# Performance work log

Hardware: AMD Instinct MI355X
Metric: run time of the kernel (lower is better)

The kernel has to match this reference:

```python
import jax, jax.numpy as jnp
import numpy as np

B, N_OBJ, N_REL = 32, 16, 64
C, H, W = 1024, 50, 50
POOL, SR = 7, 2          # roi_pool_size, sampling_ratio
SPATIAL_SCALE = 1.0      # boxes are pre-scaled to fmap coords by scale_bboxes
DIMS = [1024, 1024, 512] # lin_obj_dim
IMG = 800                # square frame -> the original's h/w swap bug is a no-op


def setup_inputs() -> dict:
    key = jax.random.key(0)
    ks = jax.random.split(key, 8)
    fmap = jax.random.normal(ks[0], (B, C, H, W), dtype=jnp.float32)
    # valid boxes in image coords: x1<x2, y1<y2, inside [0, IMG]
    xy1 = jax.random.uniform(ks[1], (B, N_OBJ, 2), minval=0.0, maxval=600.0)
    wh = jax.random.uniform(ks[2], (B, N_OBJ, 2), minval=50.0, maxval=200.0)
    bboxes = jnp.concatenate([xy1, xy1 + wh], axis=-1).astype(jnp.float32)
    num_obj = jnp.full((B,), N_OBJ, dtype=jnp.int32)
    num_rels = jnp.full((B,), N_REL, dtype=jnp.int32)
    obj_pairs = jax.random.randint(ks[3], (B, N_REL, 2), 0, N_OBJ, dtype=jnp.int32)
    s1 = 1.0 / np.sqrt(DIMS[0]).astype(np.float32)
    s2 = 1.0 / np.sqrt(DIMS[1]).astype(np.float32)
    W1 = jax.random.uniform(ks[4], (DIMS[0], DIMS[1]), minval=-s1, maxval=s1, dtype=jnp.float32)
    b1 = jax.random.uniform(ks[5], (DIMS[1],), minval=-s1, maxval=s1, dtype=jnp.float32)
    W2 = jax.random.uniform(ks[6], (DIMS[1], DIMS[2]), minval=-s2, maxval=s2, dtype=jnp.float32)
    b2 = jax.random.uniform(ks[7], (DIMS[2],), minval=-s2, maxval=s2, dtype=jnp.float32)
    return dict(frame_feature_map=fmap, bboxes=bboxes, num_obj=num_obj,
                obj_pairs=obj_pairs, num_rels=num_rels,
                frame_width=IMG, frame_height=IMG,
                W1=W1, b1=b1, W2=W2, b2=b2)


def _interp_axis(coord, size):
    # torchvision RoIAlign (aligned=False) bilinear precompute along one axis
    valid = ((coord >= -1.0) & (coord <= size)).astype(coord.dtype)
    c = jnp.maximum(coord, 0.0)
    low = jnp.floor(c).astype(jnp.int32)
    at_edge = low >= size - 1
    low = jnp.minimum(low, size - 1)
    high = jnp.minimum(low + 1, size - 1)
    l = jnp.where(at_edge, 0.0, c - low.astype(coord.dtype))
    return low, high, 1.0 - l, l, valid


def roi_align(fmap, boxes, batch_idx, pool, sr, scale):
    # fmap [B,C,H,W]; boxes [R,4] (x1,y1,x2,y2); returns [R,pool,pool,C]
    _, Cc, Hc, Wc = fmap.shape
    x1, y1, x2, y2 = (boxes[:, i] * scale for i in range(4))
    roi_w = jnp.maximum(x2 - x1, 1.0)
    roi_h = jnp.maximum(y2 - y1, 1.0)
    # sample offsets (separable): bin ph, subsample iy -> ph + (iy+0.5)/sr, in bin units
    grid = (jnp.arange(pool, dtype=fmap.dtype)[:, None]
            + (jnp.arange(sr, dtype=fmap.dtype)[None, :] + 0.5) / sr).reshape(-1)  # [pool*sr]
    ys = y1[:, None] + (roi_h / pool)[:, None] * grid[None, :]  # [R, Sy]
    xs = x1[:, None] + (roi_w / pool)[:, None] * grid[None, :]  # [R, Sx]
    yl, yh, wy0, wy1, vy = _interp_axis(ys, Hc)
    xl, xh, wx0, wx1, vx = _interp_axis(xs, Wc)
    b = batch_idx[:, None, None]

    def g(yi, xi):
        # advanced indices split by ':' -> result [R, Sy, Sx, C]
        return fmap[b, :, yi[:, :, None], xi[:, None, :]]

    val = (wy0[:, :, None, None] * (wx0[:, None, :, None] * g(yl, xl)
                                    + wx1[:, None, :, None] * g(yl, xh))
           + wy1[:, :, None, None] * (wx0[:, None, :, None] * g(yh, xl)
                                      + wx1[:, None, :, None] * g(yh, xh)))
    val = val * (vy[:, :, None, None] * vx[:, None, :, None])  # out-of-range points -> 0
    R = boxes.shape[0]
    # average the sr x sr samples per bin (count = sr*sr, as in torchvision)
    return val.reshape(R, pool, sr, pool, sr, Cc).mean(axis=(2, 4))


def reference(frame_feature_map, bboxes, num_obj, obj_pairs, num_rels,
              frame_width, frame_height, W1, b1, W2, b2):
    Bn, Nmax = bboxes.shape[:2]
    # scale_bboxes -- faithful to the original (note its im_height/im_width swap)
    im_height, im_width = frame_width, frame_height
    fh, fw = frame_feature_map.shape[-2:]
    hs = fh / (im_height * 1.0)
    ws = fw / (im_width * 1.0)
    scaled = bboxes * jnp.asarray([ws, hs, ws, hs], dtype=bboxes.dtype)
    boxes = scaled.reshape(-1, 4)                              # full counts: concat == flatten
    batch_idx = jnp.repeat(jnp.arange(Bn, dtype=jnp.int32), Nmax)
    roi = roi_align(frame_feature_map, boxes, batch_idx, POOL, SR, SPATIAL_SCALE)  # [R,7,7,C]
    # lin_obj_net: Linear+ReLU stack applied on the channel (last) dim
    h = jax.nn.relu(roi @ W1 + b1)
    h = jax.nn.relu(h @ W2 + b2)                               # [R,7,7,512]
    feat = h.mean(axis=(1, 2))                                 # AvgPool2d(7x7) -> flatten: [R,512]
    # pair_features: gather two object vectors per relation and average
    obj_off = jnp.concatenate([jnp.zeros((1,), jnp.int32),
                               jnp.cumsum(num_obj)[:-1].astype(jnp.int32)])
    idx = obj_off[:, None, None] + obj_pairs                   # [B, N_REL, 2]
    f0 = feat[idx[..., 0].reshape(-1)]
    f1 = feat[idx[..., 1].reshape(-1)]
    return 0.5 * (f0 + f1)                                     # [sum(num_rels), 512]
```

## Files before the change

kernel.cpp:

```cpp
#include <hip/hip_runtime.h>

#define DEV __device__ __forceinline__

typedef unsigned short u16;
typedef short bf16x8 __attribute__((ext_vector_type(8)));
typedef float f32x4 __attribute__((ext_vector_type(4)));

#define BB    32
#define NOBJ  16
#define NREL  64
#define CCH   1024
#define FHW   50
#define HW    2500
#define NROI  512
#define MROWS 25088
#define D1    1024
#define D2    512

DEV u16 f2bf(float f) {
  unsigned u = __float_as_uint(f);
  unsigned r = (u + 0x7FFFu + ((u >> 16) & 1u)) >> 16;
  return (u16)r;
}
DEV float bf2f(u16 h) { return __uint_as_float((unsigned)h << 16); }
DEV unsigned pk(float lo, float hi) { return (unsigned)f2bf(lo) | ((unsigned)f2bf(hi) << 16); }

using gvoid = __attribute__((address_space(1))) const void;
using svoid = __attribute__((address_space(3))) void;
DEV void gl_lds16(const void* g, void* s) {
  __builtin_amdgcn_global_load_lds((gvoid*)g, (svoid*)s, 16, 0, 0);
}

__global__ __launch_bounds__(256) void k_transpose_cast(
    const float* __restrict__ in, u16* __restrict__ out, int R, int C) {
  __shared__ float tile[64][65];
  const int b = blockIdx.z;
  const int c0 = blockIdx.x * 64;
  const int r0 = blockIdx.y * 64;
  const float* inb = in + (size_t)b * R * C;
  u16* outb = out + (size_t)b * R * C;
  const int t = threadIdx.x;

  {
    const int rr = t >> 4;
    const int cq = (t & 15) * 4;
#pragma unroll
    for (int it = 0; it < 4; ++it) {
      int rl = rr + it * 16;
      int r = r0 + rl;
      int c = c0 + cq;
      if (c + 3 < C) {
        float4 v = *reinterpret_cast<const float4*>(&inb[(size_t)r * C + c]);
        tile[rl][cq + 0] = v.x; tile[rl][cq + 1] = v.y;
        tile[rl][cq + 2] = v.z; tile[rl][cq + 3] = v.w;
      } else {
#pragma unroll
        for (int j = 0; j < 4; ++j)
          tile[rl][cq + j] = (c + j < C) ? inb[(size_t)r * C + c + j] : 0.f;
      }
    }
  }
  __syncthreads();
  {
    const int c = t >> 2;
    const int rch = (t & 3) * 8;
    if (c0 + c < C) {
#pragma unroll
      for (int half = 0; half < 2; ++half) {
        int rb = rch + half * 32;
        uint4 o;
        o.x = pk(tile[rb + 0][c], tile[rb + 1][c]);
        o.y = pk(tile[rb + 2][c], tile[rb + 3][c]);
        o.z = pk(tile[rb + 4][c], tile[rb + 5][c]);
        o.w = pk(tile[rb + 6][c], tile[rb + 7][c]);
        *reinterpret_cast<uint4*>(&outb[(size_t)(c0 + c) * R + r0 + rb]) = o;
      }
    }
  }
}

DEV void acc8(const u16* p, float w, float* a) {
  uint4 v = *reinterpret_cast<const uint4*>(p);
  a[0] = fmaf(w, bf2f((u16)(v.x & 0xffffu)), a[0]);
  a[1] = fmaf(w, bf2f((u16)(v.x >> 16)), a[1]);
  a[2] = fmaf(w, bf2f((u16)(v.y & 0xffffu)), a[2]);
  a[3] = fmaf(w, bf2f((u16)(v.y >> 16)), a[3]);
  a[4] = fmaf(w, bf2f((u16)(v.z & 0xffffu)), a[4]);
  a[5] = fmaf(w, bf2f((u16)(v.z >> 16)), a[5]);
  a[6] = fmaf(w, bf2f((u16)(v.w & 0xffffu)), a[6]);
  a[7] = fmaf(w, bf2f((u16)(v.w >> 16)), a[7]);
}

__global__ __launch_bounds__(128) void k_roi_fast(
    const u16* __restrict__ fmT, const float* __restrict__ bboxes,
    const int* __restrict__ pfw, const int* __restrict__ pfh,
    u16* __restrict__ Aout) {
  const int r = blockIdx.x;
  const int py = blockIdx.y;
  const int b = r >> 4;
  const int t = threadIdx.x;
  const int c0 = t * 8;

  __shared__ int s_lo[2][14], s_hi[2][14];
  __shared__ float s_w0[2][14], s_w1[2][14], s_v[2][14];

  int axis = -1, i = 0;
  if (t < 14) { axis = 0; i = t; }
  else if (t >= 64 && t < 78) { axis = 1; i = t - 64; }
  if (axis >= 0) {
    float fwf = (float)pfw[0], fhf = (float)pfh[0];
    float hs = (float)FHW / fwf;
    float wsc = (float)FHW / fhf;
    float v1 = bboxes[r * 4 + (axis == 0 ? 1 : 0)] * (axis == 0 ? hs : wsc);
    float v2 = bboxes[r * 4 + (axis == 0 ? 3 : 2)] * (axis == 0 ? hs : wsc);
    float ext = fmaxf(v2 - v1, 1.0f);
    float g = (float)(i >> 1) + ((i & 1) ? 0.75f : 0.25f);
    float coord = v1 + (ext / 7.0f) * g;
    float valid = (coord >= -1.0f && coord <= 50.0f) ? 1.0f : 0.0f;
    float cc = fmaxf(coord, 0.0f);
    int lo = (int)floorf(cc);
    bool edge = (lo >= FHW - 1);
    lo = min(lo, FHW - 1);
    int hi = min(lo + 1, FHW - 1);
    float l = edge ? 0.0f : (cc - (float)lo);
    s_lo[axis][i] = lo; s_hi[axis][i] = hi;
    s_w0[axis][i] = 1.0f - l; s_w1[axis][i] = l; s_v[axis][i] = valid;
  }
  __syncthreads();

  const u16* bt = fmT + (size_t)b * HW * CCH + c0;

  for (int px = 0; px < 7; ++px) {
    float a[8] = {};
#pragma unroll
    for (int s = 0; s < 4; ++s) {
      int sy = s >> 1, sx = s & 1;
      int iy = py * 2 + sy, jx = px * 2 + sx;
      int yl = s_lo[0][iy], yh = s_hi[0][iy];
      int xl = s_lo[1][jx], xh = s_hi[1][jx];
      float vv = s_v[0][iy] * s_v[1][jx];
      float wy0 = s_w0[0][iy] * vv, wy1 = s_w1[0][iy] * vv;
      float wx0 = s_w0[1][jx], wx1 = s_w1[1][jx];
      acc8(bt + (size_t)(yl * FHW + xl) * CCH, wy0 * wx0, a);
      acc8(bt + (size_t)(yl * FHW + xh) * CCH, wy0 * wx1, a);
      acc8(bt + (size_t)(yh * FHW + xl) * CCH, wy1 * wx0, a);
      acc8(bt + (size_t)(yh * FHW + xh) * CCH, wy1 * wx1, a);
    }
    u16* dst = Aout + (size_t)(r * 49 + py * 7 + px) * CCH + c0;
    uint4 o;
    o.x = pk(a[0] * 0.25f, a[1] * 0.25f);
    o.y = pk(a[2] * 0.25f, a[3] * 0.25f);
    o.z = pk(a[4] * 0.25f, a[5] * 0.25f);
    o.w = pk(a[6] * 0.25f, a[7] * 0.25f);
    *reinterpret_cast<uint4*>(dst) = o;
  }
}

__global__ __launch_bounds__(64) void k_roi_slow(
    const float* __restrict__ fmap, const float* __restrict__ bboxes,
    const int* __restrict__ pfw, const int* __restrict__ pfh,
    u16* __restrict__ Aout) {
  const int r = blockIdx.x;
  const int b = r >> 4;
  const int t = threadIdx.x;
  const int c0 = (blockIdx.y * 64 + t) * 4;

  __shared__ int s_lo[2][14], s_hi[2][14];
  __shared__ float s_w0[2][14], s_w1[2][14], s_v[2][14];

  int axis = -1, i = 0;
  if (t < 14) { axis = 0; i = t; }
  else if (t >= 32 && t < 46) { axis = 1; i = t - 32; }
  if (axis >= 0) {
    float fwf = (float)pfw[0], fhf = (float)pfh[0];
    float hs = (float)FHW / fwf;
    float wsc = (float)FHW / fhf;
    float v1 = bboxes[r * 4 + (axis == 0 ? 1 : 0)] * (axis == 0 ? hs : wsc);
    float v2 = bboxes[r * 4 + (axis == 0 ? 3 : 2)] * (axis == 0 ? hs : wsc);
    float ext = fmaxf(v2 - v1, 1.0f);
    float g = (float)(i >> 1) + ((i & 1) ? 0.75f : 0.25f);
    float coord = v1 + (ext / 7.0f) * g;
    float valid = (coord >= -1.0f && coord <= 50.0f) ? 1.0f : 0.0f;
    float cc = fmaxf(coord, 0.0f);
    int lo = (int)floorf(cc);
    bool edge = (lo >= FHW - 1);
    lo = min(lo, FHW - 1);
    int hi = min(lo + 1, FHW - 1);
    float l = edge ? 0.0f : (cc - (float)lo);
    s_lo[axis][i] = lo; s_hi[axis][i] = hi;
    s_w0[axis][i] = 1.0f - l; s_w1[axis][i] = l; s_v[axis][i] = valid;
  }
  __syncthreads();

  const float* bfc = fmap + (size_t)b * CCH * HW + (size_t)c0 * HW;

  for (int bin = 0; bin < 49; ++bin) {
    int py = bin / 7, px = bin % 7;
    float a0 = 0.f, a1 = 0.f, a2 = 0.f, a3 = 0.f;
#pragma unroll
    for (int s = 0; s < 4; ++s) {
      int sy = s >> 1, sx = s & 1;
      int iy = py * 2 + sy, jx = px * 2 + sx;
      int yl = s_lo[0][iy], yh = s_hi[0][iy];
      int xl = s_lo[1][jx], xh = s_hi[1][jx];
      float vv = s_v[0][iy] * s_v[1][jx];
      float wy0 = s_w0[0][iy] * vv, wy1 = s_w1[0][iy] * vv;
      float wx0 = s_w0[1][jx], wx1 = s_w1[1][jx];
      float w00 = wy0 * wx0, w01 = wy0 * wx1, w10 = wy1 * wx0, w11 = wy1 * wx1;
      int p00 = yl * FHW + xl, p01 = yl * FHW + xh;
      int p10 = yh * FHW + xl, p11 = yh * FHW + xh;
      a0 += w00 * bfc[0 * HW + p00] + w01 * bfc[0 * HW + p01] + w10 * bfc[0 * HW + p10] + w11 * bfc[0 * HW + p11];
      a1 += w00 * bfc[1 * HW + p00] + w01 * bfc[1 * HW + p01] + w10 * bfc[1 * HW + p10] + w11 * bfc[1 * HW + p11];
      a2 += w00 * bfc[2 * HW + p00] + w01 * bfc[2 * HW + p01] + w10 * bfc[2 * HW + p10] + w11 * bfc[2 * HW + p11];
      a3 += w00 * bfc[3 * HW + p00] + w01 * bfc[3 * HW + p01] + w10 * bfc[3 * HW + p10] + w11 * bfc[3 * HW + p11];
    }
    u16* dst = Aout + (size_t)(r * 49 + bin) * CCH + c0;
    ushort4 o;
    o.x = f2bf(a0 * 0.25f); o.y = f2bf(a1 * 0.25f);
    o.z = f2bf(a2 * 0.25f); o.w = f2bf(a3 * 0.25f);
    *reinterpret_cast<ushort4*>(dst) = o;
  }
}

template <int K, int N, int OBF>
__global__ __launch_bounds__(256) void k_gemm(
    const u16* __restrict__ A, const u16* __restrict__ Bt,
    const float* __restrict__ bias, void* __restrict__ Out) {
  __shared__ alignas(16) u16 As[128 * 32];
  __shared__ alignas(16) u16 Bs[128 * 32];
  const int t = threadIdx.x;
  const int lane = t & 63, w = t >> 6;
  const int wr = w >> 1, wc = w & 1;

  const int NT = N / 128;
  const int bid = blockIdx.x;
  const int chunk = (int)(gridDim.x >> 3);
  const int swz = (bid & 7) * chunk + (bid >> 3);
  const size_t m0 = (size_t)(swz / NT) * 128;
  const int n0 = (swz % NT) * 128;

  f32x4 acc[4][4] = {};

  const int srow = t >> 2;
  const int skc = (t & 3) * 8;

  for (int ks = 0; ks < K / 32; ++ks) {
    const int k0 = ks * 32;
    if (ks) __syncthreads();
    gl_lds16(A + (m0 + srow) * K + k0 + skc, &As[(size_t)t * 8]);
    gl_lds16(A + (m0 + 64 + srow) * K + k0 + skc, &As[(size_t)(t + 256) * 8]);
    gl_lds16(Bt + (size_t)(n0 + srow) * K + k0 + skc, &Bs[(size_t)t * 8]);
    gl_lds16(Bt + (size_t)(n0 + 64 + srow) * K + k0 + skc, &Bs[(size_t)(t + 256) * 8]);
    __syncthreads();

    const int koff = (lane >> 4) * 8;
    bf16x8 av[4], bv[4];
#pragma unroll
    for (int m = 0; m < 4; ++m)
      av[m] = *reinterpret_cast<const bf16x8*>(&As[(wr * 64 + m * 16 + (lane & 15)) * 32 + koff]);
#pragma unroll
    for (int n = 0; n < 4; ++n)
      bv[n] = *reinterpret_cast<const bf16x8*>(&Bs[(wc * 64 + n * 16 + (lane & 15)) * 32 + koff]);
#pragma unroll
    for (int m = 0; m < 4; ++m)
#pragma unroll
      for (int n = 0; n < 4; ++n)
        asm("v_mfma_f32_16x16x32_bf16 %0, %1, %2, %0"
            : "+v"(acc[m][n]) : "v"(av[m]), "v"(bv[n]));
  }
  asm volatile("s_nop 7\n\ts_nop 7\n\ts_nop 7" ::);

#pragma unroll
  for (int n = 0; n < 4; ++n) {
    int col = n0 + wc * 64 + n * 16 + (lane & 15);
    float bb = bias[col];
#pragma unroll
    for (int m = 0; m < 4; ++m) {
      size_t row0 = m0 + wr * 64 + m * 16 + (lane >> 4) * 4;
#pragma unroll
      for (int qq = 0; qq < 4; ++qq) {
        float v = fmaxf(acc[m][n][qq] + bb, 0.0f);
        if (OBF) ((u16*)Out)[(row0 + qq) * N + col] = f2bf(v);
        else     ((float*)Out)[(row0 + qq) * N + col] = v;
      }
    }
  }
}

__global__ __launch_bounds__(256) void k_mean(const u16* __restrict__ H2,
                                              float* __restrict__ feat) {
  const int r = blockIdx.x;
  const int c = threadIdx.x * 2;
  float s0 = 0.f, s1 = 0.f;
#pragma unroll
  for (int qq = 0; qq < 49; ++qq) {
    unsigned v = *reinterpret_cast<const unsigned*>(&H2[((size_t)r * 49 + qq) * D2 + c]);
    s0 += bf2f((u16)(v & 0xffffu));
    s1 += bf2f((u16)(v >> 16));
  }
  feat[(size_t)r * D2 + c] = s0 * (1.0f / 49.0f);
  feat[(size_t)r * D2 + c + 1] = s1 * (1.0f / 49.0f);
}

__global__ __launch_bounds__(256) void k_pairs(
    const float* __restrict__ feat, const int* __restrict__ num_obj,
    const int* __restrict__ pairs, float* __restrict__ out) {
  int r = blockIdx.x;
  int b = r >> 6;
  int off = 0;
  for (int i = 0; i < b; ++i) off += num_obj[i];
  int g0 = off + pairs[r * 2 + 0];
  int g1 = off + pairs[r * 2 + 1];
  for (int c = threadIdx.x; c < D2; c += 256) {
    out[(size_t)r * D2 + c] = 0.5f * (feat[(size_t)g0 * D2 + c] + feat[(size_t)g1 * D2 + c]);
  }
}

extern "C" void kernel_launch(void* const* d_in, const int* in_sizes, int n_in,
                              void* d_out, int out_size, void* d_ws, size_t ws_size,
                              hipStream_t stream) {
  const float* fmap = (const float*)d_in[0];
  const float* bboxes = (const float*)d_in[1];
  const int* num_obj = (const int*)d_in[2];
  const int* obj_pairs = (const int*)d_in[3];
  const int* pfw = (const int*)d_in[5];
  const int* pfh = (const int*)d_in[6];
  const float* W1 = (const float*)d_in[7];
  const float* b1 = (const float*)d_in[8];
  const float* W2 = (const float*)d_in[9];
  const float* b2 = (const float*)d_in[10];
  float* out = (float*)d_out;

  const size_t SZ_FMT = (size_t)BB * HW * CCH * 2;
  const size_t SZ_A   = (size_t)MROWS * D1 * 2;
  const size_t SZ_H1  = (size_t)MROWS * D1 * 2;
  const size_t SZ_W1B = (size_t)D1 * D1 * 2;
  const size_t SZ_W2B = (size_t)D1 * D2 * 2;
  const size_t SZ_FEAT = (size_t)NROI * D2 * 4;

  char* ws = (char*)d_ws;
  const bool fast = ws_size >= SZ_FMT + SZ_A + SZ_H1 + SZ_W1B + SZ_W2B + SZ_FEAT;

  u16 *fmT, *A, *H1, *W1b, *W2b, *H2b;
  float *feat;
  if (fast) {
    fmT = (u16*)ws;
    A = (u16*)(ws + SZ_FMT);
    H1 = (u16*)(ws + SZ_FMT + SZ_A);
    W1b = (u16*)(ws + SZ_FMT + SZ_A + SZ_H1);
    W2b = (u16*)(ws + SZ_FMT + SZ_A + SZ_H1 + SZ_W1B);
    feat = (float*)(ws + SZ_FMT + SZ_A + SZ_H1 + SZ_W1B + SZ_W2B);
    H2b = fmT;
  } else {
    fmT = nullptr;
    A = (u16*)ws;
    H1 = (u16*)(ws + SZ_A);
    W1b = (u16*)(ws + SZ_A + SZ_H1);
    W2b = (u16*)(ws + SZ_A + SZ_H1 + SZ_W1B);
    feat = (float*)(ws + SZ_A + SZ_H1 + SZ_W1B + SZ_W2B);
    H2b = A;
  }

  k_transpose_cast<<<dim3(16, 16, 1), 256, 0, stream>>>(W1, W1b, D1, D1);
  k_transpose_cast<<<dim3(8, 16, 1), 256, 0, stream>>>(W2, W2b, D1, D2);

  if (fast) {
    k_transpose_cast<<<dim3(40, 16, BB), 256, 0, stream>>>(fmap, fmT, CCH, HW);
    k_roi_fast<<<dim3(NROI, 7), 128, 0, stream>>>(fmT, bboxes, pfw, pfh, A);
  } else {
    k_roi_slow<<<dim3(NROI, 4), 64, 0, stream>>>(fmap, bboxes, pfw, pfh, A);
  }

  k_gemm<D1, D1, 1><<<(MROWS / 128) * (D1 / 128), 256, 0, stream>>>(A, W1b, b1, (void*)H1);
  k_gemm<D1, D2, 1><<<(MROWS / 128) * (D2 / 128), 256, 0, stream>>>(H1, W2b, b2, (void*)H2b);
  k_mean<<<NROI, 256, 0, stream>>>(H2b, feat);
  k_pairs<<<BB * NREL, 256, 0, stream>>>(feat, num_obj, obj_pairs, out);
}
```

Measured before the change: 291.0 us.

## Add 256x256 double-buffered 8-wave GEMM with swizzled LDS and remove slow ROI path

Adds a new GEMM kernel with 256x256 output tiles, 8 waves, a 64-wide K step and double-buffered dynamic LDS (128 KB). The next K tile is prefetched while MFMAs run, and LDS addresses are XOR-swizzled to avoid bank conflicts. It also uses XCD-aware block remapping and setprio around the MFMA bursts. The aim is more data reuse per tile and overlap of global loads with compute in the two large GEMMs. The fallback ROI path that avoided workspace is removed, so the code now assumes the workspace is large enough.

```diff
diff --git a/kernel.cpp b/kernel.cpp
--- a/kernel.cpp
+++ b/kernel.cpp
@@ -40,7 +40,6 @@
   const float* inb = in + (size_t)b * R * C;
   u16* outb = out + (size_t)b * R * C;
   const int t = threadIdx.x;
-
   {
     const int rr = t >> 4;
     const int cq = (t & 15) * 4;
@@ -156,69 +155,119 @@
   }
 }
 
-__global__ __launch_bounds__(64) void k_roi_slow(
-    const float* __restrict__ fmap, const float* __restrict__ bboxes,
-    const int* __restrict__ pfw, const int* __restrict__ pfh,
-    u16* __restrict__ Aout) {
-  const int r = blockIdx.x;
-  const int b = r >> 4;
+template <int K, int N, int OBF>
+__global__ __launch_bounds__(512, 2) void k_gemm8(
+    const u16* __restrict__ A, const u16* __restrict__ Bt,
+    const float* __restrict__ bias, void* __restrict__ Out) {
+  extern __shared__ char smem[];
   const int t = threadIdx.x;
-  const int c0 = (blockIdx.y * 64 + t) * 4;
-
-  __shared__ int s_lo[2][14], s_hi[2][14];
-  __shared__ float s_w0[2][14], s_w1[2][14], s_v[2][14];
-
-  int axis = -1, i = 0;
-  if (t < 14) { axis = 0; i = t; }
-  else if (t >= 32 && t < 46) { axis = 1; i = t - 32; }
-  if (axis >= 0) {
-    float fwf = (float)pfw[0], fhf = (float)pfh[0];
-    float hs = (float)FHW / fwf;
-    float wsc = (float)FHW / fhf;
-    float v1 = bboxes[r * 4 + (axis == 0 ? 1 : 0)] * (axis == 0 ? hs : wsc);
-    float v2 = bboxes[r * 4 + (axis == 0 ? 3 : 2)] * (axis == 0 ? hs : wsc);
-    float ext = fmaxf(v2 - v1, 1.0f);
-    float g = (float)(i >> 1) + ((i & 1) ? 0.75f : 0.25f);
-    float coord = v1 + (ext / 7.0f) * g;
-    float valid = (coord >= -1.0f && coord <= 50.0f) ? 1.0f : 0.0f;
-    float cc = fmaxf(coord, 0.0f);
-    int lo = (int)floorf(cc);
-    bool edge = (lo >= FHW - 1);
-    lo = min(lo, FHW - 1);
-    int hi = min(lo + 1, FHW - 1);
-    float l = edge ? 0.0f : (cc - (float)lo);
-    s_lo[axis][i] = lo; s_hi[axis][i] = hi;
-    s_w0[axis][i] = 1.0f - l; s_w1[axis][i] = l; s_v[axis][i] = valid;
-  }
-  __syncthreads();
-
-  const float* bfc = fmap + (size_t)b * CCH * HW + (size_t)c0 * HW;
-
-  for (int bin = 0; bin < 49; ++bin) {
-    int py = bin / 7, px = bin % 7;
-    float a0 = 0.f, a1 = 0.f, a2 = 0.f, a3 = 0.f;
-#pragma unroll
-    for (int s = 0; s < 4; ++s) {
-      int sy = s >> 1, sx = s & 1;
-      int iy = py * 2 + sy, jx = px * 2 + sx;
-      int yl = s_lo[0][iy], yh = s_hi[0][iy];
-      int xl = s_lo[1][jx], xh = s_hi[1][jx];
-      float vv = s_v[0][iy] * s_v[1][jx];
-      float wy0 = s_w0[0][iy] * vv, wy1 = s_w1[0][iy] * vv;
-      float wx0 = s_w0[1][jx], wx1 = s_w1[1][jx];
-      float w00 = wy0 * wx0, w01 = wy0 * wx1, w10 = wy1 * wx0, w11 = wy1 * wx1;
-      int p00 = yl * FHW + xl, p01 = yl * FHW + xh;
-      int p10 = yh * FHW + xl, p11 = yh * FHW + xh;
-      a0 += w00 * bfc[0 * HW + p00] + w01 * bfc[0 * HW + p01] + w10 * bfc[0 * HW + p10] + w11 * bfc[0 * HW + p11];
-      a1 += w00 * bfc[1 * HW + p00] + w01 * bfc[1 * HW + p01] + w10 * bfc[1 * HW + p10] + w11 * bfc[1 * HW + p11];
-      a2 += w00 * bfc[2 * HW + p00] + w01 * bfc[2 * HW + p01] + w10 * bfc[2 * HW + p10] + w11 * bfc[2 * HW + p11];
-      a3 += w00 * bfc[3 * HW + p00] + w01 * bfc[3 * HW + p01] + w10 * bfc[3 * HW + p10] + w11 * bfc[3 * HW + p11];
-    }
-    u16* dst = Aout + (size_t)(r * 49 + bin) * CCH + c0;
-    ushort4 o;
-    o.x = f2bf(a0 * 0.25f); o.y = f2bf(a1 * 0.25f);
-    o.z = f2bf(a2 * 0.25f); o.w = f2bf(a3 * 0.25f);
-    *reinterpret_cast<ushort4*>(dst) = o;
+  const int lane = t & 63;
+  const int wid = t >> 6;
+  const int wr = wid >> 2, wc = wid & 3;
+
+  const int nwg = (int)gridDim.x;
+  const int orig = (int)blockIdx.x;
+  const int xcd = orig & 7, q = nwg >> 3, r = nwg & 7;
+  const int swz = (xcd < r ? xcd * (q + 1) : r * (q + 1) + (xcd - r) * q) + (orig >> 3);
+  constexpr int GN = N / 256;
+  const size_t m0 = (size_t)(swz / GN) * 256;
+  const int n0 = (swz % GN) * 256;
+
+  constexpr int NKT = K / 64;
+
+  f32x4 acc[8][4] = {};
+
+  auto stage_quarter = [&](int bufb, int k0, int qt) {
+    const u16* src = (qt < 2) ? A : Bt;
+    const size_t rbase = (qt < 2) ? m0 : (size_t)n0;
+    const int regionBase = bufb + ((qt < 2) ? 0 : 32768);
+    const int half = qt & 1;
+#pragma unroll
+    for (int c = 0; c < 2; ++c) {
+      int P = half * 16384 + c * 8192 + t * 16;
+      int L = P ^ (((P >> 9) & 1) << 5);
+      int row = L >> 7;
+      int kb = L & 127;
+      gl_lds16(src + (rbase + row) * (size_t)K + k0 + (kb >> 1),
+               smem + regionBase + P);
+    }
+  };
+  auto lda = [&](int bufb, int mrow, int kc) -> bf16x8 {
+    int L = mrow * 128 + kc * 2;
+    int P = L ^ (((L >> 9) & 1) << 5);
+    return *reinterpret_cast<const bf16x8*>(smem + bufb + P);
+  };
+  auto ldb = [&](int bufb, int nrow, int kc) -> bf16x8 {
+    int L = nrow * 128 + kc * 2;
+    int P = L ^ (((L >> 9) & 1) << 5);
+    return *reinterpret_cast<const bf16x8*>(smem + bufb + 32768 + P);
+  };
+
+#pragma unroll
+  for (int qt = 0; qt < 4; ++qt) stage_quarter(0, 0, qt);
+  if (NKT > 1) {
+#pragma unroll
+    for (int qt = 0; qt < 4; ++qt) stage_quarter(65536, 64, qt);
+  }
+  asm volatile("s_waitcnt vmcnt(0)" ::: "memory");
+  __builtin_amdgcn_s_barrier();
+
+  for (int tt = 0; tt < NKT; ++tt) {
+    const int bb = (tt & 1) ? 65536 : 0;
+    const int nb = bb ^ 65536;
+    const bool do_stage = (tt >= 1) && (tt + 1 < NKT);
+    const int k0n = (tt + 1) * 64;
+#pragma unroll
+    for (int p = 0; p < 4; ++p) {
+      const int qm = p >> 1, qn = p & 1;
+      bf16x8 av[2][4], bv[2][2];
+#pragma unroll
+      for (int ks = 0; ks < 2; ++ks) {
+        const int kc = ks * 32 + (lane >> 4) * 8;
+#pragma unroll
+        for (int m = 0; m < 4; ++m)
+          av[ks][m] = lda(bb, wr * 128 + qm * 64 + m * 16 + (lane & 15), kc);
+#pragma unroll
+        for (int n = 0; n < 2; ++n)
+          bv[ks][n] = ldb(bb, wc * 64 + qn * 32 + n * 16 + (lane & 15), kc);
+      }
+      if (do_stage && p < 2) {
+        stage_quarter(nb, k0n, p * 2 + 0);
+        stage_quarter(nb, k0n, p * 2 + 1);
+      }
+      __builtin_amdgcn_s_barrier();
+      __builtin_amdgcn_s_setprio(1);
+#pragma unroll
+      for (int ks = 0; ks < 2; ++ks)
+#pragma unroll
+        for (int m = 0; m < 4; ++m)
+#pragma unroll
+          for (int n = 0; n < 2; ++n)
+            asm("v_mfma_f32_16x16x32_bf16 %0, %1, %2, %0"
+                : "+v"(acc[qm * 4 + m][qn * 2 + n])
+                : "v"(av[ks][m]), "v"(bv[ks][n]));
+      __builtin_amdgcn_s_setprio(0);
+      if (p == 3 && tt + 1 < NKT)
+        asm volatile("s_waitcnt vmcnt(0)" ::: "memory");
+      __builtin_amdgcn_s_barrier();
+    }
+  }
+  asm volatile("s_nop 7\n\ts_nop 7\n\ts_nop 7" ::);
+
+#pragma unroll
+  for (int nf = 0; nf < 4; ++nf) {
+    const int col = n0 + wc * 64 + nf * 16 + (lane & 15);
+    const float bbv = bias[col];
+#pragma unroll
+    for (int mf = 0; mf < 8; ++mf) {
+      const size_t row0 = m0 + wr * 128 + mf * 16 + (lane >> 4) * 4;
+#pragma unroll
+      for (int qq = 0; qq < 4; ++qq) {
+        float v = fmaxf(acc[mf][nf][qq] + bbv, 0.0f);
+        if (OBF) ((u16*)Out)[(row0 + qq) * N + col] = f2bf(v);
+        else     ((float*)Out)[(row0 + qq) * N + col] = v;
+      }
+    }
   }
 }
 
@@ -231,19 +280,15 @@
   const int t = threadIdx.x;
   const int lane = t & 63, w = t >> 6;
   const int wr = w >> 1, wc = w & 1;
-
   const int NT = N / 128;
   const int bid = blockIdx.x;
   const int chunk = (int)(gridDim.x >> 3);
   const int swz = (bid & 7) * chunk + (bid >> 3);
   const size_t m0 = (size_t)(swz / NT) * 128;
   const int n0 = (swz % NT) * 128;
-
   f32x4 acc[4][4] = {};
-
   const int srow = t >> 2;
   const int skc = (t & 3) * 8;
-
   for (int ks = 0; ks < K / 32; ++ks) {
     const int k0 = ks * 32;
     if (ks) __syncthreads();
@@ -252,7 +297,6 @@
     gl_lds16(Bt + (size_t)(n0 + srow) * K + k0 + skc, &Bs[(size_t)t * 8]);
     gl_lds16(Bt + (size_t)(n0 + 64 + srow) * K + k0 + skc, &Bs[(size_t)(t + 256) * 8]);
     __syncthreads();
-
     const int koff = (lane >> 4) * 8;
     bf16x8 av[4], bv[4];
 #pragma unroll
@@ -269,7 +313,6 @@
             : "+v"(acc[m][n]) : "v"(av[m]), "v"(bv[n]));
   }
   asm volatile("s_nop 7\n\ts_nop 7\n\ts_nop 7" ::);
-
 #pragma unroll
   for (int n = 0; n < 4; ++n) {
     int col = n0 + wc * 64 + n * 16 + (lane & 15);
@@ -339,40 +382,37 @@
   const size_t SZ_FEAT = (size_t)NROI * D2 * 4;
 
   char* ws = (char*)d_ws;
-  const bool fast = ws_size >= SZ_FMT + SZ_A + SZ_H1 + SZ_W1B + SZ_W2B + SZ_FEAT;
-
   u16 *fmT, *A, *H1, *W1b, *W2b, *H2b;
   float *feat;
-  if (fast) {
-    fmT = (u16*)ws;
-    A = (u16*)(ws + SZ_FMT);
-    H1 = (u16*)(ws + SZ_FMT + SZ_A);
-    W1b = (u16*)(ws + SZ_FMT + SZ_A + SZ_H1);
-    W2b = (u16*)(ws + SZ_FMT + SZ_A + SZ_H1 + SZ_W1B);
-    feat = (float*)(ws + SZ_FMT + SZ_A + SZ_H1 + SZ_W1B + SZ_W2B);
-    H2b = fmT;
-  } else {
-    fmT = nullptr;
-    A = (u16*)ws;
-    H1 = (u16*)(ws + SZ_A);
-    W1b = (u16*)(ws + SZ_A + SZ_H1);
-    W2b = (u16*)(ws + SZ_A + SZ_H1 + SZ_W1B);
-    feat = (float*)(ws + SZ_A + SZ_H1 + SZ_W1B + SZ_W2B);
-    H2b = A;
-  }
+  fmT = (u16*)ws;
+  A = (u16*)(ws + SZ_FMT);
+  H1 = (u16*)(ws + SZ_FMT + SZ_A);
+  W1b = (u16*)(ws + SZ_FMT + SZ_A + SZ_H1);
+  W2b = (u16*)(ws + SZ_FMT + SZ_A + SZ_H1 + SZ_W1B);
+  feat = (float*)(ws + SZ_FMT + SZ_A + SZ_H1 + SZ_W1B + SZ_W2B);
+  H2b = fmT;
+
+  bool useNew = true;
+  if (hipFuncSetAttribute((const void*)k_gemm8<D1, D1, 1>,
+                          hipFuncAttributeMaxDynamicSharedMemorySize, 131072) != hipSuccess)
+    useNew = false;
+  if (hipFuncSetAttribute((const void*)k_gemm8<D1, D2, 1>,
+                          hipFuncAttributeMaxDynamicSharedMemorySize, 131072) != hipSuccess)
+    useNew = false;
 
   k_transpose_cast<<<dim3(16, 16, 1), 256, 0, stream>>>(W1, W1b, D1, D1);
   k_transpose_cast<<<dim3(8, 16, 1), 256, 0, stream>>>(W2, W2b, D1, D2);
 
-  if (fast) {
-    k_transpose_cast<<<dim3(40, 16, BB), 256, 0, stream>>>(fmap, fmT, CCH, HW);
-    k_roi_fast<<<dim3(NROI, 7), 128, 0, stream>>>(fmT, bboxes, pfw, pfh, A);
+  k_transpose_cast<<<dim3(40, 16, BB), 256, 0, stream>>>(fmap, fmT, CCH, HW);
+  k_roi_fast<<<dim3(NROI, 7), 128, 0, stream>>>(fmT, bboxes, pfw, pfh, A);
+
+  if (useNew) {
+    k_gemm8<D1, D1, 1><<<(MROWS / 256) * (D1 / 256), 512, 131072, stream>>>(A, W1b, b1, (void*)H1);
+    k_gemm8<D1, D2, 1><<<(MROWS / 256) * (D2 / 256), 512, 131072, stream>>>(H1, W2b, b2, (void*)H2b);
   } else {
-    k_roi_slow<<<dim3(NROI, 4), 64, 0, stream>>>(fmap, bboxes, pfw, pfh, A);
-  }
-
-  k_gemm<D1, D1, 1><<<(MROWS / 128) * (D1 / 128), 256, 0, stream>>>(A, W1b, b1, (void*)H1);
-  k_gemm<D1, D2, 1><<<(MROWS / 128) * (D2 / 128), 256, 0, stream>>>(H1, W2b, b2, (void*)H2b);
+    k_gemm<D1, D1, 1><<<(MROWS / 128) * (D1 / 128), 256, 0, stream>>>(A, W1b, b1, (void*)H1);
+    k_gemm<D1, D2, 1><<<(MROWS / 128) * (D2 / 128), 256, 0, stream>>>(H1, W2b, b2, (void*)H2b);
+  }
   k_mean<<<NROI, 256, 0, stream>>>(H2b, feat);
   k_pairs<<<BB * NREL, 256, 0, stream>>>(feat, num_obj, obj_pairs, out);
 }
```

Result: slower. 337.7 us (+16.1%).
